# Kernel optimization log

Measured on AMD Instinct MI355X. Metric: run time of the kernel, lower is better.

The kernel has to match this reference:

```python
import jax, jax.numpy as jnp
import numpy as np

ALPHA, ETA, THETA = 0.999, 0.6, 0.05
EPS = 1e-12  # torch F.normalize eps

def silu(x):
    return x * jax.nn.sigmoid(x)

def l2norm(x):
    # torch.nn.functional.normalize(x) : p=2, dim=1
    n = jnp.linalg.norm(x, axis=1, keepdims=True)
    return x / jnp.maximum(n, EPS)

def mlp(params, x):
    # layers[0]: Linear(16,32)+SiLU ; layers[1]: Linear(32,16)+SiLU
    W0, b0, W1, b1 = params
    h = silu(x @ W0.T + b0)
    return silu(h @ W1.T + b1)

def setup_inputs() -> dict:
    key = jax.random.key(0)
    ks = jax.random.split(key, 8)
    N, D, H = 1048576, 16, 32
    def w(k, shape):
        fan_in = shape[1]
        return jax.random.normal(k, shape, jnp.float32) / np.float32(np.sqrt(fan_in))
    return {
        'X':  jax.random.normal(ks[0], (N, D), jnp.float32),
        'W0': w(ks[1], (H, D)),
        'b0': jnp.zeros((H,), jnp.float32),
        'W1': w(ks[2], (D, H)),
        'b1': jnp.zeros((D,), jnp.float32),
        'WK': w(ks[3], (D, D)),
        'WV': w(ks[4], (D, D)),
        'WQ': w(ks[5], (D, D)),
    }

def reference(X, W0, b0, W1, b1, WK, WV, WQ):
    # ---- update(X): test-time gradient write into the tiny MLP memory ----
    x = jax.lax.stop_gradient(X)            # X.detach()
    v = jax.lax.stop_gradient(silu(x @ WV.T))     # with torch.no_grad()
    q = l2norm(silu(x @ WQ.T))              # normalize(silu(Q(x)))

    def loss_fn(p):
        y = mlp(p, q)
        return jnp.mean((y - v) ** 2)

    g = jax.grad(loss_fn)((W0, b0, W1, b1))
    # surprise starts empty -> zeros; surprise = eta*0 - theta*g = -theta*g
    # update_params = alpha*base.detach() + surprise.detach()
    new_params = tuple(jax.lax.stop_gradient(ALPHA * p - THETA * gi)
                       for p, gi in zip((W0, b0, W1, b1), g))

    # ---- retrieve(X, new_params): key-value read ----
    # note order differs from update: silu(normalize(Q(X)))
    r_in = silu(l2norm(X @ WQ.T))
    return mlp(new_params, r_in)
```

## Files before the change

### kernel.cpp

```cpp
#include <hip/hip_runtime.h>
#include <hip/hip_bf16.h>

typedef __attribute__((ext_vector_type(8))) __bf16 bf16x8;
typedef __attribute__((ext_vector_type(4))) float f32x4;
typedef __attribute__((ext_vector_type(16))) float f32x16;

union U8 { bf16x8 v; unsigned u[4]; uint2 d[2]; };

#define ALPHA 0.999f
#define THETA 0.05f

#define K1_BLOCKS 1536
#define K3_BLOCKS 1536

#define RREC 100
#define F_DY 0
#define F_H  16
#define F_Q  48
#define F_DH 64
#define WAVE_HALFS (32*RREC)
#define K1_SMEM_BYTES 28672

#define R3 100
#define Q_HI 0
#define Q_LO 16
#define H_HI 32
#define H_LO 64

#if __has_builtin(__builtin_amdgcn_rcpf)
#define RCPF(x) __builtin_amdgcn_rcpf(x)
#else
#define RCPF(x) (1.f/(x))
#endif
#if __has_builtin(__builtin_amdgcn_rsqf)
#define RSQF(x) __builtin_amdgcn_rsqf(x)
#else
#define RSQF(x) (1.f/sqrtf(x))
#endif

__device__ __forceinline__ float sigmoidf_(float z){ return RCPF(1.f + __expf(-z)); }

__device__ __forceinline__ unsigned pk2_(float a, float b){
  union { __bf16 h[2]; unsigned u; } x; x.h[0]=(__bf16)a; x.h[1]=(__bf16)b; return x.u;
}
__device__ __forceinline__ float upks_(unsigned u, int s){
  return s ? __uint_as_float(u & 0xffff0000u) : __uint_as_float(u << 16);
}
__device__ __forceinline__ void splitpk_(float a, float b, unsigned &uh, unsigned &ul){
  unsigned h = pk2_(a,b);
  float ah = __uint_as_float(h << 16);
  float bh = __uint_as_float(h & 0xffff0000u);
  uh = h; ul = pk2_(a - ah, b - bh);
}
__device__ __forceinline__ void load_split8_(const float* p, U8 &H, U8 &L){
  const float4 u0 = *(const float4*)p;
  const float4 u1 = *(const float4*)(p+4);
  splitpk_(u0.x,u0.y,H.u[0],L.u[0]); splitpk_(u0.z,u0.w,H.u[1],L.u[1]);
  splitpk_(u1.x,u1.y,H.u[2],L.u[2]); splitpk_(u1.z,u1.w,H.u[3],L.u[3]);
}
__device__ __forceinline__ void pack8f_(const float* p, U8 &A){
  const float4 u0 = *(const float4*)p;
  const float4 u1 = *(const float4*)(p+4);
  A.u[0]=pk2_(u0.x,u0.y); A.u[1]=pk2_(u0.z,u0.w); A.u[2]=pk2_(u1.x,u1.y); A.u[3]=pk2_(u1.z,u1.w);
}

__global__ __launch_bounds__(256, 3)
void k1_grad(const float* __restrict__ X,
             const float* __restrict__ W0, const float* __restrict__ b0,
             const float* __restrict__ W1, const float* __restrict__ b1,
             const float* __restrict__ WV, const float* __restrict__ WQ,
             float* __restrict__ wsPart, int N)
{
  __shared__ __align__(16) unsigned char smem_raw[K1_SMEM_BYTES];
  const int tid = threadIdx.x;
  const int w = tid >> 6, l = tid & 63;
  const int row = l & 31, hi = l >> 5;
  const int c16 = l & 15, g16 = l >> 4;
  __bf16* WB = (__bf16*)smem_raw + w*WAVE_HALFS;

  bf16x8 ones;
  #pragma unroll
  for (int i=0;i<8;++i) ones[i] = (__bf16)1.f;

  U8 aWVQ, aW0p;
  pack8f_((row < 16) ? (WV + row*16 + hi*8) : (WQ + (row-16)*16 + hi*8), aWVQ);
  pack8f_(W0 + row*16 + hi*8, aW0p);

  f32x4 accW[4] = {};
  f32x4 accB1 = {}, accB0a = {}, accB0b = {};

  const int nb = N >> 6;
  const int tw = K1_BLOCKS*4;
  const int gw = blockIdx.x*4 + w;
  const int iters = (nb + tw - 1) / tw;

  for (int it = 0; it < iters; ++it) {
    const int batch = gw + it*tw;
    if (batch < nb) {
      const float* xb = X + (size_t)batch*1024;

      #pragma unroll
      for (int hf=0; hf<2; ++hf){
        const float* xh = xb + hf*512;
        __bf16* R = WB + row*RREC;

        U8 bX; pack8f_(xh + row*16 + hi*8, bX);
        f32x16 c1;
        #pragma unroll
        for (int i=0;i<16;++i) c1[i] = 0.f;
        c1 = __builtin_amdgcn_mfma_f32_32x32x16_bf16(aWVQ.v, bX.v, c1, 0,0,0);
        unsigned vvp[4];
        #pragma unroll
        for (int j=0;j<4;++j){
          float a = c1[2*j],  sa = a*sigmoidf_(a);
          float b = c1[2*j+1],sb = b*sigmoidf_(b);
          vvp[j] = pk2_(sa, sb);
        }
        float qv[8]; float n2 = 0.f;
        #pragma unroll
        for (int r=0;r<8;++r){
          float s = c1[8+r]; float t = s*sigmoidf_(s);
          qv[r] = t; n2 = fmaf(t,t,n2);
        }
        n2 += __shfl_xor(n2, 32);
        const float inv = RSQF(fmaxf(n2, 1e-24f));
        *(uint2*)(R + F_Q + 4*hi)     = make_uint2(pk2_(qv[0]*inv,qv[1]*inv), pk2_(qv[2]*inv,qv[3]*inv));
        *(uint2*)(R + F_Q + 8 + 4*hi) = make_uint2(pk2_(qv[4]*inv,qv[5]*inv), pk2_(qv[6]*inv,qv[7]*inv));

        U8 bq;
        { const __bf16* p = R + F_Q + hi*8;
          bq.d[0] = *(const uint2*)p; bq.d[1] = *(const uint2*)(p+4); }
        f32x16 c2;
        { const float4 bA = *(const float4*)(b0 + 4*hi);
          const float4 bB = *(const float4*)(b0 + 8 + 4*hi);
          const float4 bC = *(const float4*)(b0 + 16 + 4*hi);
          const float4 bD = *(const float4*)(b0 + 24 + 4*hi);
          c2[0]=bA.x;c2[1]=bA.y;c2[2]=bA.z;c2[3]=bA.w;
          c2[4]=bB.x;c2[5]=bB.y;c2[6]=bB.z;c2[7]=bB.w;
          c2[8]=bC.x;c2[9]=bC.y;c2[10]=bC.z;c2[11]=bC.w;
          c2[12]=bD.x;c2[13]=bD.y;c2[14]=bD.z;c2[15]=bD.w; }
        c2 = __builtin_amdgcn_mfma_f32_32x32x16_bf16(aW0p.v, bq.v, c2, 0,0,0);
        unsigned hpk[8], dshp[8];
        #pragma unroll
        for (int j=0;j<8;++j){
          float sa = c2[2*j],   sga = sigmoidf_(sa);
          float sb = c2[2*j+1], sgb = sigmoidf_(sb);
          hpk[j]  = pk2_(sa*sga, sb*sgb);
          dshp[j] = pk2_(sga*fmaf(sa,1.f-sga,1.f), sgb*fmaf(sb,1.f-sgb,1.f));
        }
        *(uint2*)(R + F_H + 4*hi)      = make_uint2(hpk[0],hpk[1]);
        *(uint2*)(R + F_H + 8 + 4*hi)  = make_uint2(hpk[2],hpk[3]);
        *(uint2*)(R + F_H + 16 + 4*hi) = make_uint2(hpk[4],hpk[5]);
        *(uint2*)(R + F_H + 24 + 4*hi) = make_uint2(hpk[6],hpk[7]);

        U8 a1, a2;
        #pragma unroll
        for (int i=0;i<4;++i){ a1.u[i]=0; a2.u[i]=0; }
        if (row < 16) pack8f_(W1 + row*32 + hi*8, a1);
        else          pack8f_(W1 + (row-16)*32 + 16 + hi*8, a2);
        U8 bhlo, bhhi;
        { const __bf16* p = R + F_H + hi*8;
          bhlo.d[0] = *(const uint2*)p; bhlo.d[1] = *(const uint2*)(p+4);
          const __bf16* p2 = R + F_H + 16 + hi*8;
          bhhi.d[0] = *(const uint2*)p2; bhhi.d[1] = *(const uint2*)(p2+4); }
        f32x16 c3;
        { const float4 bA = *(const float4*)(b1 + 4*hi);
          const float4 bB = *(const float4*)(b1 + 8 + 4*hi);
          c3[0]=bA.x;c3[1]=bA.y;c3[2]=bA.z;c3[3]=bA.w;
          c3[4]=bB.x;c3[5]=bB.y;c3[6]=bB.z;c3[7]=bB.w;
          #pragma unroll
          for (int i=8;i<16;++i) c3[i]=0.f; }
        c3 = __builtin_amdgcn_mfma_f32_32x32x16_bf16(a1.v, bhlo.v, c3, 0,0,0);
        c3 = __builtin_amdgcn_mfma_f32_32x32x16_bf16(a2.v, bhhi.v, c3, 0,0,0);
        unsigned dypk[4];
        #pragma unroll
        for (int j=0;j<4;++j){
          float d2[2];
          #pragma unroll
          for (int e=0;e<2;++e){
            int r = 2*j+e;
            float s = c3[r] + c3[r+8];
            float sg = sigmoidf_(s);
            float y = s*sg;
            float ds = sg * fmaf(s, 1.f - sg, 1.f);
            d2[e] = (y - upks_(vvp[r>>1], r&1)) * ds;
          }
          dypk[j] = pk2_(d2[0], d2[1]);
        }
        *(uint2*)(R + F_DY + 4*hi)     = make_uint2(dypk[0],dypk[1]);
        *(uint2*)(R + F_DY + 8 + 4*hi) = make_uint2(dypk[2],dypk[3]);

        U8 aT;
        { float t0 = W1[(hi*8+0)*32 + row], t1 = W1[(hi*8+1)*32 + row];
          float t2 = W1[(hi*8+2)*32 + row], t3 = W1[(hi*8+3)*32 + row];
          float t4 = W1[(hi*8+4)*32 + row], t5 = W1[(hi*8+5)*32 + row];
          float t6 = W1[(hi*8+6)*32 + row], t7 = W1[(hi*8+7)*32 + row];
          aT.u[0]=pk2_(t0,t1); aT.u[1]=pk2_(t2,t3); aT.u[2]=pk2_(t4,t5); aT.u[3]=pk2_(t6,t7); }
        U8 bdy;
        { const __bf16* p = R + F_DY + hi*8;
          bdy.d[0] = *(const uint2*)p; bdy.d[1] = *(const uint2*)(p+4); }
        f32x16 c4;
        #pragma unroll
        for (int i=0;i<16;++i) c4[i]=0.f;
        c4 = __builtin_amdgcn_mfma_f32_32x32x16_bf16(aT.v, bdy.v, c4, 0,0,0);
        unsigned dhpk[8];
        #pragma unroll
        for (int j=0;j<8;++j){
          float d0 = c4[2*j]   * upks_(dshp[j],0);
          float d1 = c4[2*j+1] * upks_(dshp[j],1);
          dhpk[j] = pk2_(d0,d1);
        }
        *(uint2*)(R + F_DH + 4*hi)      = make_uint2(dhpk[0],dhpk[1]);
        *(uint2*)(R + F_DH + 8 + 4*hi)  = make_uint2(dhpk[2],dhpk[3]);
        *(uint2*)(R + F_DH + 16 + 4*hi) = make_uint2(dhpk[4],dhpk[5]);
        *(uint2*)(R + F_DH + 24 + 4*hi) = make_uint2(dhpk[6],dhpk[7]);

        const __bf16* gbase = WB + (g16*8)*RREC + c16;
        {
          bf16x8 fdy, fh0, fh1;
          #pragma unroll
          for (int i=0;i<8;++i){
            const __bf16* pr = gbase + i*RREC;
            fdy[i] = pr[F_DY];
            fh0[i] = pr[F_H];
            fh1[i] = pr[F_H + 16];
          }
          accW[0] = __builtin_amdgcn_mfma_f32_16x16x32_bf16(fdy, fh0, accW[0], 0,0,0);
          accW[1] = __builtin_amdgcn_mfma_f32_16x16x32_bf16(fdy, fh1, accW[1], 0,0,0);
          accB1   = __builtin_amdgcn_mfma_f32_16x16x32_bf16(fdy, ones, accB1, 0,0,0);
        }
        {
          bf16x8 fd0, fd1, fq;
          #pragma unroll
          for (int i=0;i<8;++i){
            const __bf16* pr = gbase + i*RREC;
            fd0[i] = pr[F_DH];
            fd1[i] = pr[F_DH + 16];
            fq[i]  = pr[F_Q];
          }
          accW[2] = __builtin_amdgcn_mfma_f32_16x16x32_bf16(fd0, fq, accW[2], 0,0,0);
          accW[3] = __builtin_amdgcn_mfma_f32_16x16x32_bf16(fd1, fq, accW[3], 0,0,0);
          accB0a  = __builtin_amdgcn_mfma_f32_16x16x32_bf16(fd0, ones, accB0a, 0,0,0);
          accB0b  = __builtin_amdgcn_mfma_f32_16x16x32_bf16(fd1, ones, accB0b, 0,0,0);
        }
      }
    }
  }

  __syncthreads();
  float* red = (float*)smem_raw;
  #pragma unroll
  for (int r=0;r<4;++r){
    red[w*1792 + 0*256 + l*4 + r] = accW[0][r];
    red[w*1792 + 1*256 + l*4 + r] = accW[1][r];
    red[w*1792 + 2*256 + l*4 + r] = accB1[r];
    red[w*1792 + 3*256 + l*4 + r] = accW[2][r];
    red[w*1792 + 4*256 + l*4 + r] = accW[3][r];
    red[w*1792 + 5*256 + l*4 + r] = accB0a[r];
    red[w*1792 + 6*256 + l*4 + r] = accB0b[r];
  }
  __syncthreads();
  for (int s = tid; s < 1792; s += 256){
    float sum = red[s] + red[1792+s] + red[2*1792+s] + red[3*1792+s];
    wsPart[(size_t)blockIdx.x*1792 + s] = sum;
  }
}

__global__ void k2a_reduce(const float* __restrict__ wsPart, float* __restrict__ tmp)
{
  const int s = blockIdx.x*256 + threadIdx.x;
  const int c = blockIdx.y;
  float g = 0.f;
  #pragma unroll 8
  for (int j=0;j<96;++j) g += wsPart[(size_t)(c*96+j)*1792 + s];
  tmp[(size_t)c*1792 + s] = g;
}

__global__ void k2b_reduce(const float* __restrict__ tmp,
                           const float* __restrict__ W0, const float* __restrict__ b0,
                           const float* __restrict__ W1, const float* __restrict__ b1,
                           float* __restrict__ P, float scale)
{
  int s = blockIdx.x*256 + threadIdx.x;
  if (s >= 1792) return;
  float g = 0.f;
  #pragma unroll
  for (int c=0;c<16;++c) g += tmp[(size_t)c*1792 + s];
  g *= scale;
  int a = s >> 8, l = (s >> 2) & 63, r = s & 3;
  int m = ((l>>4)<<2) + r, n = l & 15;
  if (a==0)      P[544 + m*32 + n]       = ALPHA*W1[m*32+n]        - THETA*g;
  else if (a==1) P[544 + m*32 + 16 + n]  = ALPHA*W1[m*32+16+n]     - THETA*g;
  else if (a==2){ if (n==0) P[1056 + m]  = ALPHA*b1[m]             - THETA*g; }
  else if (a==3) P[m*16 + n]             = ALPHA*W0[m*16+n]        - THETA*g;
  else if (a==4) P[(16+m)*16 + n]        = ALPHA*W0[(16+m)*16+n]   - THETA*g;
  else if (a==5){ if (n==0) P[512 + m]   = ALPHA*b0[m]             - THETA*g; }
  else           { if (n==0) P[512+16+m] = ALPHA*b0[16+m]          - THETA*g; }
}

__global__ __launch_bounds__(256, 3)
void k3_retrieve(const float* __restrict__ X, const float* __restrict__ WQ,
                 const float* __restrict__ P, float* __restrict__ out, int N)
{
  __shared__ __align__(16) __bf16 smem[4*64*R3];
  const int tid = threadIdx.x;
  const int w = tid >> 6, l = tid & 63;
  const int g = l >> 4, c = l & 15;
  __bf16* WB = smem + w*64*R3;
  const f32x4 zz = {0.f,0.f,0.f,0.f};

  U8 aQh, aQl, aW0h[2], aW0l[2], aW1h, aW1l;
  #pragma unroll
  for (int i=0;i<4;++i){
    aQh.u[i]=aQl.u[i]=0;
    aW0h[0].u[i]=aW0l[0].u[i]=0; aW0h[1].u[i]=aW0l[1].u[i]=0;
  }
  if (g < 2){
    load_split8_(WQ + c*16 + g*8, aQh, aQl);
    #pragma unroll
    for (int T=0;T<2;++T) load_split8_(P + (16*T + c)*16 + g*8, aW0h[T], aW0l[T]);
  }
  load_split8_(P + 544 + c*32 + g*8, aW1h, aW1l);
  const f32x4 b0q0 = *(const f32x4*)(P + 512 + 4*g);
  const f32x4 b0q1 = *(const f32x4*)(P + 528 + 4*g);
  const f32x4 b1q  = *(const f32x4*)(P + 1056 + 4*g);

  const int nb = N >> 6;
  const int tw = K3_BLOCKS*4;
  const int gw = blockIdx.x*4 + w;
  const int iters = (nb + tw - 1) / tw;

  for (int it=0; it<iters; ++it){
    const int batch = gw + it*tw;
    if (batch < nb){
      const float* xb = X + (size_t)batch*1024;

      #pragma unroll
      for (int t=0;t<4;++t){
        U8 bXh, bXl;
        if (g < 2){ load_split8_(xb + (16*t + c)*16 + g*8, bXh, bXl); }
        else { bXh.u[0]=bXh.u[1]=bXh.u[2]=bXh.u[3]=0; bXl=bXh; }
        f32x4 s = __builtin_amdgcn_mfma_f32_16x16x32_bf16(aQl.v, bXh.v, zz, 0,0,0);
        s = __builtin_amdgcn_mfma_f32_16x16x32_bf16(aQh.v, bXl.v, s, 0,0,0);
        s = __builtin_amdgcn_mfma_f32_16x16x32_bf16(aQh.v, bXh.v, s, 0,0,0);
        float n2 = 0.f;
        #pragma unroll
        for (int r=0;r<4;++r) n2 = fmaf(s[r], s[r], n2);
        n2 += __shfl_xor(n2, 16);
        n2 += __shfl_xor(n2, 32);
        const float inv = RSQF(fmaxf(n2, 1e-24f));
        float qv[4];
        #pragma unroll
        for (int r=0;r<4;++r){ float z = s[r]*inv; qv[r] = z * sigmoidf_(z); }
        unsigned qh0,ql0,qh1,ql1;
        splitpk_(qv[0],qv[1],qh0,ql0); splitpk_(qv[2],qv[3],qh1,ql1);
        __bf16* R = WB + (16*t + c)*R3;
        *(uint2*)(R + Q_HI + 4*g) = make_uint2(qh0,qh1);
        *(uint2*)(R + Q_LO + 4*g) = make_uint2(ql0,ql1);
      }

      #pragma unroll
      for (int t=0;t<4;++t){
        U8 bqh, bql;
        if (g < 2){
          const __bf16* p = WB + (16*t + c)*R3;
          bqh.d[0] = *(const uint2*)(p + Q_HI + 8*g); bqh.d[1] = *(const uint2*)(p + Q_HI + 8*g + 4);
          bql.d[0] = *(const uint2*)(p + Q_LO + 8*g); bql.d[1] = *(const uint2*)(p + Q_LO + 8*g + 4);
        } else {
          bqh.u[0]=bqh.u[1]=bqh.u[2]=bqh.u[3]=0; bql=bqh;
        }
        #pragma unroll
        for (int T=0;T<2;++T){
          f32x4 sh = __builtin_amdgcn_mfma_f32_16x16x32_bf16(aW0l[T].v, bqh.v, T? b0q1 : b0q0, 0,0,0);
          sh = __builtin_amdgcn_mfma_f32_16x16x32_bf16(aW0h[T].v, bql.v, sh, 0,0,0);
          sh = __builtin_amdgcn_mfma_f32_16x16x32_bf16(aW0h[T].v, bqh.v, sh, 0,0,0);
          float hv[4];
          #pragma unroll
          for (int r=0;r<4;++r){ float s = sh[r]; hv[r] = s * sigmoidf_(s); }
          unsigned hh0,hl0,hh1,hl1;
          splitpk_(hv[0],hv[1],hh0,hl0); splitpk_(hv[2],hv[3],hh1,hl1);
          __bf16* R = WB + (16*t + c)*R3;
          *(uint2*)(R + H_HI + 16*T + 4*g) = make_uint2(hh0,hh1);
          *(uint2*)(R + H_LO + 16*T + 4*g) = make_uint2(hl0,hl1);
        }
      }

      #pragma unroll
      for (int t=0;t<4;++t){
        U8 bhh, bhl;
        const __bf16* p = WB + (16*t + c)*R3;
        bhh.d[0] = *(const uint2*)(p + H_HI + 8*g); bhh.d[1] = *(const uint2*)(p + H_HI + 8*g + 4);
        bhl.d[0] = *(const uint2*)(p + H_LO + 8*g); bhl.d[1] = *(const uint2*)(p + H_LO + 8*g + 4);
        f32x4 sy = __builtin_amdgcn_mfma_f32_16x16x32_bf16(aW1l.v, bhh.v, b1q, 0,0,0);
        sy = __builtin_amdgcn_mfma_f32_16x16x32_bf16(aW1h.v, bhl.v, sy, 0,0,0);
        sy = __builtin_amdgcn_mfma_f32_16x16x32_bf16(aW1h.v, bhh.v, sy, 0,0,0);
        float4 o;
        o.x = sy[0]*sigmoidf_(sy[0]);
        o.y = sy[1]*sigmoidf_(sy[1]);
        o.z = sy[2]*sigmoidf_(sy[2]);
        o.w = sy[3]*sigmoidf_(sy[3]);
        *(float4*)(out + ((size_t)batch*64 + 16*t + c)*16 + 4*g) = o;
      }
    }
  }
}

extern "C" void kernel_launch(void* const* d_in, const int* in_sizes, int n_in,
                              void* d_out, int out_size, void* d_ws, size_t ws_size,
                              hipStream_t stream)
{
  const float* X  = (const float*)d_in[0];
  const float* W0 = (const float*)d_in[1];
  const float* b0 = (const float*)d_in[2];
  const float* W1 = (const float*)d_in[3];
  const float* b1 = (const float*)d_in[4];
  const float* WV = (const float*)d_in[6];
  const float* WQ = (const float*)d_in[7];
  float* ws   = (float*)d_ws;
  float* P    = ws;
  float* part = ws + 2048;
  float* tmp  = part + (size_t)K1_BLOCKS*1792;

  const int N = in_sizes[0] / 16;
  const float scale = 2.f / (16.f * (float)N);

  k1_grad<<<dim3(K1_BLOCKS), dim3(256), 0, stream>>>(X, W0, b0, W1, b1, WV, WQ, part, N);
  k2a_reduce<<<dim3(7,16), dim3(256), 0, stream>>>(part, tmp);
  k2b_reduce<<<dim3(7), dim3(256), 0, stream>>>(tmp, W0, b0, W1, b1, P, scale);
  k3_retrieve<<<dim3(K3_BLOCKS), dim3(256), 0, stream>>>(X, WQ, P, (float*)d_out, N);
}
```

Measured before the change: 94.62 us.

## Switch retrieve kernel to 32x32x16 MFMA tiles processing 32 rows per sub-batch

Rewrites the retrieve kernel to use 32x32x16 bf16 MFMA instead of 16x16x32. The old version left half the lanes idle (g>=2 zero-padded) for the 16-wide K dimensions. The new mapping packs the hi/lo bf16 split terms into the extra M rows and sums the two halves of the accumulator. This uses every lane, halves the shared-memory scratch, and processes 32 rows per sub-batch with fused stages. The trade-off is a more complex lane mapping and larger f32x16 accumulators, which raise register pressure.

```diff
diff --git a/kernel.cpp b/kernel.cpp
--- a/kernel.cpp
+++ b/kernel.cpp
@@ -302,28 +302,24 @@
 void k3_retrieve(const float* __restrict__ X, const float* __restrict__ WQ,
                  const float* __restrict__ P, float* __restrict__ out, int N)
 {
-  __shared__ __align__(16) __bf16 smem[4*64*R3];
+  __shared__ __align__(16) __bf16 smem[4*32*R3];
   const int tid = threadIdx.x;
   const int w = tid >> 6, l = tid & 63;
-  const int g = l >> 4, c = l & 15;
-  __bf16* WB = smem + w*64*R3;
-  const f32x4 zz = {0.f,0.f,0.f,0.f};
-
-  U8 aQh, aQl, aW0h[2], aW0l[2], aW1h, aW1l;
-  #pragma unroll
-  for (int i=0;i<4;++i){
-    aQh.u[i]=aQl.u[i]=0;
-    aW0h[0].u[i]=aW0l[0].u[i]=0; aW0h[1].u[i]=aW0l[1].u[i]=0;
+  const int col = l & 31, hi = l >> 5;
+  __bf16* WB = smem + w*32*R3;
+  __bf16* R = WB + col*R3;
+
+  U8 aQ, aW0h_, aW0l_, a1, a2;
+  {
+    U8 Hh, Ll;
+    load_split8_(WQ + (col & 15)*16 + hi*8, Hh, Ll);
+    aQ = (col < 16) ? Hh : Ll;
+    load_split8_(P + col*16 + hi*8, aW0h_, aW0l_);
+    load_split8_(P + 544 + (col & 15)*32 + hi*8, Hh, Ll);
+    a1 = (col < 16) ? Hh : Ll;
+    load_split8_(P + 544 + (col & 15)*32 + 16 + hi*8, Hh, Ll);
+    a2 = (col < 16) ? Hh : Ll;
   }
-  if (g < 2){
-    load_split8_(WQ + c*16 + g*8, aQh, aQl);
-    #pragma unroll
-    for (int T=0;T<2;++T) load_split8_(P + (16*T + c)*16 + g*8, aW0h[T], aW0l[T]);
-  }
-  load_split8_(P + 544 + c*32 + g*8, aW1h, aW1l);
-  const f32x4 b0q0 = *(const f32x4*)(P + 512 + 4*g);
-  const f32x4 b0q1 = *(const f32x4*)(P + 528 + 4*g);
-  const f32x4 b1q  = *(const f32x4*)(P + 1056 + 4*g);
 
   const int nb = N >> 6;
   const int tw = K3_BLOCKS*4;
@@ -333,73 +329,93 @@
   for (int it=0; it<iters; ++it){
     const int batch = gw + it*tw;
     if (batch < nb){
-      const float* xb = X + (size_t)batch*1024;
-
       #pragma unroll
-      for (int t=0;t<4;++t){
+      for (int sb=0; sb<2; ++sb){
+        const float* xs = X + (size_t)batch*1024 + sb*512;
+
         U8 bXh, bXl;
-        if (g < 2){ load_split8_(xb + (16*t + c)*16 + g*8, bXh, bXl); }
-        else { bXh.u[0]=bXh.u[1]=bXh.u[2]=bXh.u[3]=0; bXl=bXh; }
-        f32x4 s = __builtin_amdgcn_mfma_f32_16x16x32_bf16(aQl.v, bXh.v, zz, 0,0,0);
-        s = __builtin_amdgcn_mfma_f32_16x16x32_bf16(aQh.v, bXl.v, s, 0,0,0);
-        s = __builtin_amdgcn_mfma_f32_16x16x32_bf16(aQh.v, bXh.v, s, 0,0,0);
-        float n2 = 0.f;
-        #pragma unroll
-        for (int r=0;r<4;++r) n2 = fmaf(s[r], s[r], n2);
-        n2 += __shfl_xor(n2, 16);
+        load_split8_(xs + col*16 + hi*8, bXh, bXl);
+        f32x16 c1;
+        #pragma unroll
+        for (int i=0;i<16;++i) c1[i]=0.f;
+        c1 = __builtin_amdgcn_mfma_f32_32x32x16_bf16(aQ.v, bXh.v, c1, 0,0,0);
+        c1 = __builtin_amdgcn_mfma_f32_32x32x16_bf16(aQ.v, bXl.v, c1, 0,0,0);
+        float sv[8]; float n2 = 0.f;
+        #pragma unroll
+        for (int r=0;r<8;++r){ sv[r] = c1[r] + c1[r+8]; n2 = fmaf(sv[r],sv[r],n2); }
         n2 += __shfl_xor(n2, 32);
         const float inv = RSQF(fmaxf(n2, 1e-24f));
-        float qv[4];
-        #pragma unroll
-        for (int r=0;r<4;++r){ float z = s[r]*inv; qv[r] = z * sigmoidf_(z); }
-        unsigned qh0,ql0,qh1,ql1;
-        splitpk_(qv[0],qv[1],qh0,ql0); splitpk_(qv[2],qv[3],qh1,ql1);
-        __bf16* R = WB + (16*t + c)*R3;
-        *(uint2*)(R + Q_HI + 4*g) = make_uint2(qh0,qh1);
-        *(uint2*)(R + Q_LO + 4*g) = make_uint2(ql0,ql1);
-      }
-
-      #pragma unroll
-      for (int t=0;t<4;++t){
+        unsigned qh[4], ql[4];
+        #pragma unroll
+        for (int j=0;j<4;++j){
+          float z0 = sv[2*j]*inv,   z1 = sv[2*j+1]*inv;
+          float q0 = z0*sigmoidf_(z0), q1 = z1*sigmoidf_(z1);
+          splitpk_(q0,q1,qh[j],ql[j]);
+        }
+        *(uint2*)(R + Q_HI + 4*hi)     = make_uint2(qh[0],qh[1]);
+        *(uint2*)(R + Q_HI + 8 + 4*hi) = make_uint2(qh[2],qh[3]);
+        *(uint2*)(R + Q_LO + 4*hi)     = make_uint2(ql[0],ql[1]);
+        *(uint2*)(R + Q_LO + 8 + 4*hi) = make_uint2(ql[2],ql[3]);
+
         U8 bqh, bql;
-        if (g < 2){
-          const __bf16* p = WB + (16*t + c)*R3;
-          bqh.d[0] = *(const uint2*)(p + Q_HI + 8*g); bqh.d[1] = *(const uint2*)(p + Q_HI + 8*g + 4);
-          bql.d[0] = *(const uint2*)(p + Q_LO + 8*g); bql.d[1] = *(const uint2*)(p + Q_LO + 8*g + 4);
-        } else {
-          bqh.u[0]=bqh.u[1]=bqh.u[2]=bqh.u[3]=0; bql=bqh;
-        }
-        #pragma unroll
-        for (int T=0;T<2;++T){
-          f32x4 sh = __builtin_amdgcn_mfma_f32_16x16x32_bf16(aW0l[T].v, bqh.v, T? b0q1 : b0q0, 0,0,0);
-          sh = __builtin_amdgcn_mfma_f32_16x16x32_bf16(aW0h[T].v, bql.v, sh, 0,0,0);
-          sh = __builtin_amdgcn_mfma_f32_16x16x32_bf16(aW0h[T].v, bqh.v, sh, 0,0,0);
-          float hv[4];
+        { const __bf16* p = R + Q_HI + hi*8;
+          bqh.d[0]=*(const uint2*)p; bqh.d[1]=*(const uint2*)(p+4);
+          const __bf16* p2 = R + Q_LO + hi*8;
+          bql.d[0]=*(const uint2*)p2; bql.d[1]=*(const uint2*)(p2+4); }
+        f32x16 c2;
+        { const float4 bA = *(const float4*)(P + 512 + 4*hi);
+          const float4 bB = *(const float4*)(P + 512 + 8 + 4*hi);
+          const float4 bC = *(const float4*)(P + 512 + 16 + 4*hi);
+          const float4 bD = *(const float4*)(P + 512 + 24 + 4*hi);
+          c2[0]=bA.x;c2[1]=bA.y;c2[2]=bA.z;c2[3]=bA.w;
+          c2[4]=bB.x;c2[5]=bB.y;c2[6]=bB.z;c2[7]=bB.w;
+          c2[8]=bC.x;c2[9]=bC.y;c2[10]=bC.z;c2[11]=bC.w;
+          c2[12]=bD.x;c2[13]=bD.y;c2[14]=bD.z;c2[15]=bD.w; }
+        c2 = __builtin_amdgcn_mfma_f32_32x32x16_bf16(aW0h_.v, bqh.v, c2, 0,0,0);
+        c2 = __builtin_amdgcn_mfma_f32_32x32x16_bf16(aW0h_.v, bql.v, c2, 0,0,0);
+        c2 = __builtin_amdgcn_mfma_f32_32x32x16_bf16(aW0l_.v, bqh.v, c2, 0,0,0);
+        unsigned hh[8], hl[8];
+        #pragma unroll
+        for (int j=0;j<8;++j){
+          float s0 = c2[2*j], s1 = c2[2*j+1];
+          float h0 = s0*sigmoidf_(s0), h1 = s1*sigmoidf_(s1);
+          splitpk_(h0,h1,hh[j],hl[j]);
+        }
+        *(uint2*)(R + H_HI + 4*hi)      = make_uint2(hh[0],hh[1]);
+        *(uint2*)(R + H_HI + 8 + 4*hi)  = make_uint2(hh[2],hh[3]);
+        *(uint2*)(R + H_HI + 16 + 4*hi) = make_uint2(hh[4],hh[5]);
+        *(uint2*)(R + H_HI + 24 + 4*hi) = make_uint2(hh[6],hh[7]);
+        *(uint2*)(R + H_LO + 4*hi)      = make_uint2(hl[0],hl[1]);
+        *(uint2*)(R + H_LO + 8 + 4*hi)  = make_uint2(hl[2],hl[3]);
+        *(uint2*)(R + H_LO + 16 + 4*hi) = make_uint2(hl[4],hl[5]);
+        *(uint2*)(R + H_LO + 24 + 4*hi) = make_uint2(hl[6],hl[7]);
+
+        U8 bhh0, bhh1, bhl0, bhl1;
+        { const __bf16* p;
+          p = R + H_HI + hi*8;      bhh0.d[0]=*(const uint2*)p; bhh0.d[1]=*(const uint2*)(p+4);
+          p = R + H_HI + 16 + hi*8; bhh1.d[0]=*(const uint2*)p; bhh1.d[1]=*(const uint2*)(p+4);
+          p = R + H_LO + hi*8;      bhl0.d[0]=*(const uint2*)p; bhl0.d[1]=*(const uint2*)(p+4);
+          p = R + H_LO + 16 + hi*8; bhl1.d[0]=*(const uint2*)p; bhl1.d[1]=*(const uint2*)(p+4); }
+        f32x16 c3;
+        { const float4 bA = *(const float4*)(P + 1056 + 4*hi);
+          const float4 bB = *(const float4*)(P + 1056 + 8 + 4*hi);
+          c3[0]=bA.x;c3[1]=bA.y;c3[2]=bA.z;c3[3]=bA.w;
+          c3[4]=bB.x;c3[5]=bB.y;c3[6]=bB.z;c3[7]=bB.w;
           #pragma unroll
-          for (int r=0;r<4;++r){ float s = sh[r]; hv[r] = s * sigmoidf_(s); }
-          unsigned hh0,hl0,hh1,hl1;
-          splitpk_(hv[0],hv[1],hh0,hl0); splitpk_(hv[2],hv[3],hh1,hl1);
-          __bf16* R = WB + (16*t + c)*R3;
-          *(uint2*)(R + H_HI + 16*T + 4*g) = make_uint2(hh0,hh1);
-          *(uint2*)(R + H_LO + 16*T + 4*g) = make_uint2(hl0,hl1);
-        }
-      }
-
-      #pragma unroll
-      for (int t=0;t<4;++t){
-        U8 bhh, bhl;
-        const __bf16* p = WB + (16*t + c)*R3;
-        bhh.d[0] = *(const uint2*)(p + H_HI + 8*g); bhh.d[1] = *(const uint2*)(p + H_HI + 8*g + 4);
-        bhl.d[0] = *(const uint2*)(p + H_LO + 8*g); bhl.d[1] = *(const uint2*)(p + H_LO + 8*g + 4);
-        f32x4 sy = __builtin_amdgcn_mfma_f32_16x16x32_bf16(aW1l.v, bhh.v, b1q, 0,0,0);
-        sy = __builtin_amdgcn_mfma_f32_16x16x32_bf16(aW1h.v, bhl.v, sy, 0,0,0);
-        sy = __builtin_amdgcn_mfma_f32_16x16x32_bf16(aW1h.v, bhh.v, sy, 0,0,0);
-        float4 o;
-        o.x = sy[0]*sigmoidf_(sy[0]);
-        o.y = sy[1]*sigmoidf_(sy[1]);
-        o.z = sy[2]*sigmoidf_(sy[2]);
-        o.w = sy[3]*sigmoidf_(sy[3]);
-        *(float4*)(out + ((size_t)batch*64 + 16*t + c)*16 + 4*g) = o;
+          for (int i=8;i<16;++i) c3[i]=0.f; }
+        c3 = __builtin_amdgcn_mfma_f32_32x32x16_bf16(a1.v, bhh0.v, c3, 0,0,0);
+        c3 = __builtin_amdgcn_mfma_f32_32x32x16_bf16(a2.v, bhh1.v, c3, 0,0,0);
+        c3 = __builtin_amdgcn_mfma_f32_32x32x16_bf16(a1.v, bhl0.v, c3, 0,0,0);
+        c3 = __builtin_amdgcn_mfma_f32_32x32x16_bf16(a2.v, bhl1.v, c3, 0,0,0);
+        float oo[8];
+        #pragma unroll
+        for (int r=0;r<8;++r){
+          float s = c3[r] + c3[r+8];
+          oo[r] = s * sigmoidf_(s);
+        }
+        const size_t xrow = (size_t)batch*64 + sb*32 + col;
+        *(float4*)(out + xrow*16 + 4*hi)     = make_float4(oo[0],oo[1],oo[2],oo[3]);
+        *(float4*)(out + xrow*16 + 8 + 4*hi) = make_float4(oo[4],oo[5],oo[6],oo[7]);
       }
     }
   }
```

Result: faster. 91.42 us (-3.4%).
